# Optimization experiments

Hardware: AMD Instinct MI355X
Metric: run time of the kernel (lower is better)

## Reference

```python
import jax, jax.numpy as jnp
import numpy as np

NUM_SEGMENTS = 100000  # number of cycle slots (max cycle id + 1)


def setup_inputs() -> dict:
    key = jax.random.key(0)
    k1, k2, k3 = jax.random.split(key, 3)
    x = jax.random.randint(k1, (100000,), 0, 22, dtype=jnp.int64)
    atom_to_cycle = jax.random.randint(k2, (2, 600000), 0, NUM_SEGMENTS, dtype=jnp.int64)
    emb_weight = jax.random.normal(k3, (22, 128), dtype=jnp.float32)  # Embedding(22, hidden_dim)
    return {"x": x, "atom_to_cycle": atom_to_cycle, "emb_weight": emb_weight}


def reference(x, atom_to_cycle, emb_weight):
    # x: [N] int atom codes; atom_to_cycle: [2, E]; emb_weight: [22, D]
    h = emb_weight[x]                       # [N, D] embedding lookup
    gathered = h[atom_to_cycle[0]]          # [E, D] gather by atom index
    # scatter_sum over cycle ids -> [NUM_SEGMENTS, D]
    out = jax.ops.segment_sum(gathered, atom_to_cycle[1], num_segments=NUM_SEGMENTS)
    return out
```

## Files before the change

### kernel.cpp

```cpp
#include <hip/hip_runtime.h>
#include <stdint.h>

#define KCODES 22
#define KW     12

typedef int   int4v   __attribute__((ext_vector_type(4)));
typedef float float4v __attribute__((ext_vector_type(4)));

#define BSHIFT   8
#define BROWS    256
#define MAXBUCK  1024
#define EPT2     8
#define CHUNK2   2048
#define CAP      32
#define BCAP     4096
#define EPT      8
#define CHUNK    2048

__global__ __launch_bounds__(256) void bin_dense(
        const int* __restrict__ a2c, const int* __restrict__ x,
        uint16_t* __restrict__ cntm, uint16_t* __restrict__ bins,
        int E, int nbuck, int nchunk) {
    __shared__ uint32_t lcnt[MAXBUCK];
    const int tid = threadIdx.x;
    const int cb  = blockIdx.x;
    for (int b = tid; b < nbuck; b += 256) lcnt[b] = 0;
    __syncthreads();

    const int base = cb * CHUNK2 + tid * EPT2;
    int atoms[EPT2] __attribute__((aligned(16)));
    int cycs[EPT2]  __attribute__((aligned(16)));
    if (((E & 3) == 0) && (base + EPT2 <= E)) {
#pragma unroll
        for (int q = 0; q < EPT2 / 4; ++q) {
            *(int4v*)(atoms + 4 * q) = __builtin_nontemporal_load((const int4v*)(a2c + base) + q);
            *(int4v*)(cycs + 4 * q)  = __builtin_nontemporal_load((const int4v*)(a2c + E + base) + q);
        }
    } else {
#pragma unroll
        for (int j = 0; j < EPT2; ++j) {
            int ei = base + j;
            atoms[j] = (ei < E) ? a2c[ei] : 0;
            cycs[j]  = (ei < E) ? a2c[E + ei] : -1;
        }
    }

#pragma unroll
    for (int j = 0; j < EPT2; ++j) {
        if (cycs[j] >= 0) {
            uint32_t code = (uint32_t)x[atoms[j]];
            uint32_t b    = (uint32_t)cycs[j] >> BSHIFT;
            uint32_t rk   = atomicAdd(&lcnt[b], 1u);
            uint16_t val  = (uint16_t)((((uint32_t)cycs[j] & (BROWS - 1)) << 5) | code);
            if (rk < CAP)
                bins[((size_t)b * nchunk + cb) * CAP + rk] = val;
        }
    }
    __syncthreads();

    for (int b = tid; b < nbuck; b += 256)
        cntm[(size_t)b * nchunk + cb] = (uint16_t)lcnt[b];
}

__global__ __launch_bounds__(256) void hist_expand2(
        const uint16_t* __restrict__ cntm, const uint16_t* __restrict__ bins,
        const float* __restrict__ emb, float* __restrict__ out,
        int num_seg, int nchunk) {
    __shared__ uint32_t hist[BROWS * KW];
    __shared__ uint16_t lc[512];
    const int tid = threadIdx.x;
    const int b   = blockIdx.x;
    const int d4  = tid & 31;
    const int sub = tid >> 5;

    float4v e[KCODES];
#pragma unroll
    for (int k = 0; k < KCODES; ++k)
        e[k] = ((const float4v*)emb)[k * 32 + d4];

    for (int i = tid; i < BROWS * KW; i += 256) hist[i] = 0;
    for (int i = tid; i < nchunk; i += 256) lc[i] = cntm[(size_t)b * nchunk + i];
    __syncthreads();

    const uint16_t* bb = bins + (size_t)b * nchunk * CAP;
    for (int i = tid; i < nchunk; i += 256) {
        int c = lc[i]; if (c > CAP) c = CAP;
        const uint16_t* cell = bb + (size_t)i * CAP;
        for (int j = 0; j < c; ++j) {
            uint32_t v = cell[j];
            atomicAdd(&hist[(v >> 5) * KW + ((v & 31u) >> 1)], 1u << ((v & 1u) << 4));
        }
    }
    __syncthreads();

    for (int r = sub; r < BROWS; r += 8) {
        int cyc = b * BROWS + r;
        if (cyc >= num_seg) break;
        const uint4* hrow = (const uint4*)&hist[r * KW];
        uint4 w0 = hrow[0], w1 = hrow[1], w2 = hrow[2];
        uint32_t wv[12] = {w0.x, w0.y, w0.z, w0.w,
                           w1.x, w1.y, w1.z, w1.w,
                           w2.x, w2.y, w2.z, w2.w};
        float4v acc = (float4v)(0.f);
#pragma unroll
        for (int w = 0; w < 11; ++w) {
            float c0 = (float)(wv[w] & 0xFFFFu);
            float c1 = (float)(wv[w] >> 16);
            float4v e0 = e[2 * w], e1 = e[2 * w + 1];
            acc.x = fmaf(c1, e1.x, fmaf(c0, e0.x, acc.x));
            acc.y = fmaf(c1, e1.y, fmaf(c0, e0.y, acc.y));
            acc.z = fmaf(c1, e1.z, fmaf(c0, e0.z, acc.z));
            acc.w = fmaf(c1, e1.w, fmaf(c0, e0.w, acc.w));
        }
        __builtin_nontemporal_store(acc, &((float4v*)out)[(size_t)cyc * 32 + d4]);
    }
}

__global__ __launch_bounds__(256) void bin_edges(
        const int* __restrict__ a2c, const int* __restrict__ x,
        uint32_t* __restrict__ gcur, uint16_t* __restrict__ binsA,
        int E, int nbuck) {
    __shared__ uint32_t lcnt[MAXBUCK];
    __shared__ uint32_t lbase[MAXBUCK];
    const int tid = threadIdx.x;
    for (int b = tid; b < nbuck; b += 256) lcnt[b] = 0;
    __syncthreads();

    const int base = blockIdx.x * CHUNK + tid * EPT;
    int atoms[EPT] __attribute__((aligned(16)));
    int cycs[EPT]  __attribute__((aligned(16)));
    if (((E & 3) == 0) && (base + EPT <= E)) {
        *(int4v*)(atoms + 0) = __builtin_nontemporal_load((const int4v*)(a2c + base));
        *(int4v*)(atoms + 4) = __builtin_nontemporal_load((const int4v*)(a2c + base) + 1);
        *(int4v*)(cycs + 0)  = __builtin_nontemporal_load((const int4v*)(a2c + E + base));
        *(int4v*)(cycs + 4)  = __builtin_nontemporal_load((const int4v*)(a2c + E + base) + 1);
    } else {
#pragma unroll
        for (int j = 0; j < EPT; ++j) {
            int ei = base + j;
            atoms[j] = (ei < E) ? a2c[ei] : 0;
            cycs[j]  = (ei < E) ? a2c[E + ei] : -1;
        }
    }

    uint16_t val[EPT], bk[EPT], rk[EPT];
#pragma unroll
    for (int j = 0; j < EPT; ++j) {
        if (cycs[j] >= 0) {
            uint32_t code = (uint32_t)x[atoms[j]];
            uint32_t b    = (uint32_t)cycs[j] >> BSHIFT;
            bk[j]  = (uint16_t)b;
            rk[j]  = (uint16_t)atomicAdd(&lcnt[b], 1u);
            val[j] = (uint16_t)((((uint32_t)cycs[j] & (BROWS - 1)) << 5) | code);
        } else {
            bk[j] = 0xFFFFu;
        }
    }
    __syncthreads();

    for (int b = tid; b < nbuck; b += 256) {
        uint32_t c = lcnt[b];
        lbase[b] = c ? atomicAdd(&gcur[b], c) : 0u;
    }
    __syncthreads();

#pragma unroll
    for (int j = 0; j < EPT; ++j) {
        if (bk[j] != 0xFFFFu) {
            uint32_t idx = lbase[bk[j]] + rk[j];
            if (idx < BCAP)
                binsA[(size_t)bk[j] * BCAP + idx] = val[j];
        }
    }
}

__global__ __launch_bounds__(256) void hist_expand(
        const uint32_t* __restrict__ gcur, const uint16_t* __restrict__ binsA,
        const float* __restrict__ emb, float* __restrict__ out, int num_seg) {
    __shared__ uint32_t hist[BROWS * KW];
    const int tid = threadIdx.x;
    const int b   = blockIdx.x;
    const int d4  = tid & 31;
    const int sub = tid >> 5;

    float4v e[KCODES];
#pragma unroll
    for (int k = 0; k < KCODES; ++k)
        e[k] = ((const float4v*)emb)[k * 32 + d4];

    for (int i = tid; i < BROWS * KW; i += 256) hist[i] = 0;
    __syncthreads();

    int n = gcur[b]; if (n > BCAP) n = BCAP;
    const uint16_t* bb = binsA + (size_t)b * BCAP;
    for (int i = tid; i < n; i += 256) {
        uint32_t v = bb[i];
        atomicAdd(&hist[(v >> 5) * KW + ((v & 31u) >> 1)], 1u << ((v & 1u) << 4));
    }
    __syncthreads();

    for (int r = sub; r < BROWS; r += 8) {
        int cyc = b * BROWS + r;
        if (cyc >= num_seg) break;
        const uint4* hrow = (const uint4*)&hist[r * KW];
        uint4 w0 = hrow[0], w1 = hrow[1], w2 = hrow[2];
        uint32_t wv[12] = {w0.x, w0.y, w0.z, w0.w,
                           w1.x, w1.y, w1.z, w1.w,
                           w2.x, w2.y, w2.z, w2.w};
        float4v acc = (float4v)(0.f);
#pragma unroll
        for (int w = 0; w < 11; ++w) {
            float c0 = (float)(wv[w] & 0xFFFFu);
            float c1 = (float)(wv[w] >> 16);
            float4v e0 = e[2 * w], e1 = e[2 * w + 1];
            acc.x = fmaf(c1, e1.x, fmaf(c0, e0.x, acc.x));
            acc.y = fmaf(c1, e1.y, fmaf(c0, e0.y, acc.y));
            acc.z = fmaf(c1, e1.z, fmaf(c0, e0.z, acc.z));
            acc.w = fmaf(c1, e1.w, fmaf(c0, e0.w, acc.w));
        }
        __builtin_nontemporal_store(acc, &((float4v*)out)[(size_t)cyc * 32 + d4]);
    }
}

__global__ void zero_out_f4(float4* __restrict__ out, int n4) {
    int i = blockIdx.x * blockDim.x + threadIdx.x;
    if (i < n4) out[i] = make_float4(0.f, 0.f, 0.f, 0.f);
}

__global__ void scatter_edges(const int* __restrict__ a2c,
                              const int* __restrict__ x,
                              const float* __restrict__ emb,
                              float* __restrict__ out, int E) {
    int t = blockIdx.x * blockDim.x + threadIdx.x;
    int e = t >> 5;
    int d = (t & 31) * 4;
    if (e < E) {
        int atom = a2c[e];
        int cyc  = a2c[E + e];
        int code = x[atom];
        const float4 ev = ((const float4*)emb)[code * 32 + (d >> 2)];
        float* o = out + (size_t)cyc * 128 + d;
        atomicAdd(o + 0, ev.x);
        atomicAdd(o + 1, ev.y);
        atomicAdd(o + 2, ev.z);
        atomicAdd(o + 3, ev.w);
    }
}

extern "C" void kernel_launch(void* const* d_in, const int* in_sizes, int n_in,
                              void* d_out, int out_size, void* d_ws, size_t ws_size,
                              hipStream_t stream) {
    const int*   x    = (const int*)d_in[0];
    const int*   a2c  = (const int*)d_in[1];
    const float* emb  = (const float*)d_in[2];
    float*       out  = (float*)d_out;

    const int E       = in_sizes[1] / 2;
    const int D       = in_sizes[2] / KCODES;
    const int num_seg = out_size / D;

    const int nbuck  = (num_seg + BROWS - 1) >> BSHIFT;
    const int nchunk = (E + CHUNK2 - 1) / CHUNK2;

    const size_t cntm_bytes = (size_t)nbuck * nchunk * sizeof(uint16_t);
    const size_t bins_off   = (cntm_bytes + 65535) & ~(size_t)65535;
    const size_t need_dense = bins_off + (size_t)nbuck * nchunk * CAP * sizeof(uint16_t);
    const size_t curA_bytes = (size_t)nbuck * sizeof(uint32_t);
    const size_t binsA_off  = (curA_bytes + 65535) & ~(size_t)65535;
    const size_t need_A     = binsA_off + (size_t)nbuck * BCAP * sizeof(uint16_t);

    if (nbuck <= MAXBUCK && nchunk <= 512 && ws_size >= need_dense) {
        uint16_t* cntm = (uint16_t*)d_ws;
        uint16_t* bins = (uint16_t*)((char*)d_ws + bins_off);
        bin_dense<<<nchunk, 256, 0, stream>>>(a2c, x, cntm, bins, E, nbuck, nchunk);
        hist_expand2<<<nbuck, 256, 0, stream>>>(cntm, bins, emb, out, num_seg, nchunk);
    } else if (nbuck <= MAXBUCK && ws_size >= need_A) {
        uint32_t* gcur  = (uint32_t*)d_ws;
        uint16_t* binsA = (uint16_t*)((char*)d_ws + binsA_off);
        (void)hipMemsetAsync(gcur, 0, curA_bytes, stream);
        int blocks1 = (E + CHUNK - 1) / CHUNK;
        bin_edges<<<blocks1, 256, 0, stream>>>(a2c, x, gcur, binsA, E, nbuck);
        hist_expand<<<nbuck, 256, 0, stream>>>(gcur, binsA, emb, out, num_seg);
    } else {
        int n4 = out_size / 4;
        zero_out_f4<<<(n4 + 255) / 256, 256, 0, stream>>>((float4*)out, n4);
        long long threads = (long long)E * 32;
        int blocks = (int)((threads + 255) / 256);
        scatter_edges<<<blocks, 256, 0, stream>>>(a2c, x, emb, out, E);
    }
    (void)n_in; (void)D;
}
```

Measured before the change: 97.28 us.

## Stage bins in LDS and write 64-byte cells with inline counts

The binning kernel now collects each bucket's entries in a shared-memory cell whose first slot holds the count, then writes whole cells to global memory as coalesced 16-byte stores. The separate count matrix goes away. The histogram kernel reads each cell with uint4 loads and an unrolled count-guarded chain instead of scalar 16-bit loads. This is meant to replace scattered 2-byte global writes and reads with wide coalesced transfers. In exchange it always writes full 64-byte cells, lowers per-cell capacity by one, and raises LDS use in bin_dense.

```diff
diff --git a/kernel.cpp b/kernel.cpp
--- a/kernel.cpp
+++ b/kernel.cpp
@@ -9,19 +9,21 @@
 
 #define BSHIFT   8
 #define BROWS    256
+#define DBUCK    512
 #define MAXBUCK  1024
 #define EPT2     8
 #define CHUNK2   2048
-#define CAP      32
+#define CAPW     32
 #define BCAP     4096
 #define EPT      8
 #define CHUNK    2048
 
 __global__ __launch_bounds__(256) void bin_dense(
         const int* __restrict__ a2c, const int* __restrict__ x,
-        uint16_t* __restrict__ cntm, uint16_t* __restrict__ bins,
+        uint16_t* __restrict__ bins,
         int E, int nbuck, int nchunk) {
-    __shared__ uint32_t lcnt[MAXBUCK];
+    __shared__ uint32_t lcnt[DBUCK];
+    __shared__ uint16_t lcell[DBUCK * CAPW];
     const int tid = threadIdx.x;
     const int cb  = blockIdx.x;
     for (int b = tid; b < nbuck; b += 256) lcnt[b] = 0;
@@ -51,23 +53,31 @@
             uint32_t code = (uint32_t)x[atoms[j]];
             uint32_t b    = (uint32_t)cycs[j] >> BSHIFT;
             uint32_t rk   = atomicAdd(&lcnt[b], 1u);
-            uint16_t val  = (uint16_t)((((uint32_t)cycs[j] & (BROWS - 1)) << 5) | code);
-            if (rk < CAP)
-                bins[((size_t)b * nchunk + cb) * CAP + rk] = val;
-        }
-    }
-    __syncthreads();
-
-    for (int b = tid; b < nbuck; b += 256)
-        cntm[(size_t)b * nchunk + cb] = (uint16_t)lcnt[b];
+            if (rk < CAPW - 1)
+                lcell[b * CAPW + 1 + rk] =
+                    (uint16_t)((((uint32_t)cycs[j] & (BROWS - 1)) << 5) | code);
+        }
+    }
+    __syncthreads();
+
+    for (int b = tid; b < nbuck; b += 256) {
+        uint32_t c = lcnt[b];
+        lcell[b * CAPW] = (uint16_t)(c < CAPW ? c : (CAPW - 1));
+    }
+    __syncthreads();
+
+    const int nseg = nbuck * 4;
+    for (int s = tid; s < nseg; s += 256) {
+        int b = s >> 2, seg = s & 3;
+        ((uint4*)bins)[((size_t)b * nchunk + cb) * 4 + seg] = ((const uint4*)lcell)[s];
+    }
 }
 
 __global__ __launch_bounds__(256) void hist_expand2(
-        const uint16_t* __restrict__ cntm, const uint16_t* __restrict__ bins,
+        const uint16_t* __restrict__ bins,
         const float* __restrict__ emb, float* __restrict__ out,
         int num_seg, int nchunk) {
     __shared__ uint32_t hist[BROWS * KW];
-    __shared__ uint16_t lc[512];
     const int tid = threadIdx.x;
     const int b   = blockIdx.x;
     const int d4  = tid & 31;
@@ -79,18 +89,59 @@
         e[k] = ((const float4v*)emb)[k * 32 + d4];
 
     for (int i = tid; i < BROWS * KW; i += 256) hist[i] = 0;
-    for (int i = tid; i < nchunk; i += 256) lc[i] = cntm[(size_t)b * nchunk + i];
-    __syncthreads();
-
-    const uint16_t* bb = bins + (size_t)b * nchunk * CAP;
+    __syncthreads();
+
+#define H(v) atomicAdd(&hist[((v) >> 5) * KW + (((v) & 31u) >> 1)], 1u << (((v) & 1u) << 4))
+    const uint4* cells = (const uint4*)bins;
     for (int i = tid; i < nchunk; i += 256) {
-        int c = lc[i]; if (c > CAP) c = CAP;
-        const uint16_t* cell = bb + (size_t)i * CAP;
-        for (int j = 0; j < c; ++j) {
-            uint32_t v = cell[j];
-            atomicAdd(&hist[(v >> 5) * KW + ((v & 31u) >> 1)], 1u << ((v & 1u) << 4));
-        }
-    }
+        const uint4* cp = cells + ((size_t)b * nchunk + i) * 4;
+        uint4 q0 = cp[0];
+        int c = (int)(q0.x & 0xFFFFu);
+        if (c > 0) {
+            uint32_t v;
+            v = q0.x >> 16;     H(v);
+            if (c > 1) { v = q0.y & 0xFFFFu; H(v); }
+            if (c > 2) { v = q0.y >> 16;     H(v); }
+            if (c > 3) { v = q0.z & 0xFFFFu; H(v); }
+            if (c > 4) { v = q0.z >> 16;     H(v); }
+            if (c > 5) { v = q0.w & 0xFFFFu; H(v); }
+            if (c > 6) { v = q0.w >> 16;     H(v); }
+            if (c > 7) {
+                uint4 q1 = cp[1];
+                v = q1.x & 0xFFFFu; H(v);
+                if (c > 8)  { v = q1.x >> 16;     H(v); }
+                if (c > 9)  { v = q1.y & 0xFFFFu; H(v); }
+                if (c > 10) { v = q1.y >> 16;     H(v); }
+                if (c > 11) { v = q1.z & 0xFFFFu; H(v); }
+                if (c > 12) { v = q1.z >> 16;     H(v); }
+                if (c > 13) { v = q1.w & 0xFFFFu; H(v); }
+                if (c > 14) { v = q1.w >> 16;     H(v); }
+                if (c > 15) {
+                    uint4 q2 = cp[2];
+                    v = q2.x & 0xFFFFu; H(v);
+                    if (c > 16) { v = q2.x >> 16;     H(v); }
+                    if (c > 17) { v = q2.y & 0xFFFFu; H(v); }
+                    if (c > 18) { v = q2.y >> 16;     H(v); }
+                    if (c > 19) { v = q2.z & 0xFFFFu; H(v); }
+                    if (c > 20) { v = q2.z >> 16;     H(v); }
+                    if (c > 21) { v = q2.w & 0xFFFFu; H(v); }
+                    if (c > 22) { v = q2.w >> 16;     H(v); }
+                    if (c > 23) {
+                        uint4 q3 = cp[3];
+                        v = q3.x & 0xFFFFu; H(v);
+                        if (c > 24) { v = q3.x >> 16;     H(v); }
+                        if (c > 25) { v = q3.y & 0xFFFFu; H(v); }
+                        if (c > 26) { v = q3.y >> 16;     H(v); }
+                        if (c > 27) { v = q3.z & 0xFFFFu; H(v); }
+                        if (c > 28) { v = q3.z >> 16;     H(v); }
+                        if (c > 29) { v = q3.w & 0xFFFFu; H(v); }
+                        if (c > 30) { v = q3.w >> 16;     H(v); }
+                    }
+                }
+            }
+        }
+    }
+#undef H
     __syncthreads();
 
     for (int r = sub; r < BROWS; r += 8) {
@@ -262,18 +313,17 @@
     const int nbuck  = (num_seg + BROWS - 1) >> BSHIFT;
     const int nchunk = (E + CHUNK2 - 1) / CHUNK2;
 
-    const size_t cntm_bytes = (size_t)nbuck * nchunk * sizeof(uint16_t);
-    const size_t bins_off   = (cntm_bytes + 65535) & ~(size_t)65535;
-    const size_t need_dense = bins_off + (size_t)nbuck * nchunk * CAP * sizeof(uint16_t);
+    const size_t need_dense = (size_t)nbuck * nchunk * CAPW * sizeof(uint16_t);
     const size_t curA_bytes = (size_t)nbuck * sizeof(uint32_t);
     const size_t binsA_off  = (curA_bytes + 65535) & ~(size_t)65535;
     const size_t need_A     = binsA_off + (size_t)nbuck * BCAP * sizeof(uint16_t);
 
-    if (nbuck <= MAXBUCK && nchunk <= 512 && ws_size >= need_dense) {
-        uint16_t* cntm = (uint16_t*)d_ws;
-        uint16_t* bins = (uint16_t*)((char*)d_ws + bins_off);
-        bin_dense<<<nchunk, 256, 0, stream>>>(a2c, x, cntm, bins, E, nbuck, nchunk);
-        hist_expand2<<<nbuck, 256, 0, stream>>>(cntm, bins, emb, out, num_seg, nchunk);
+    const bool ws_aligned = (((uintptr_t)d_ws) & 15) == 0;
+
+    if (nbuck <= DBUCK && ws_aligned && ws_size >= need_dense) {
+        uint16_t* bins = (uint16_t*)d_ws;
+        bin_dense<<<nchunk, 256, 0, stream>>>(a2c, x, bins, E, nbuck, nchunk);
+        hist_expand2<<<nbuck, 256, 0, stream>>>(bins, emb, out, num_seg, nchunk);
     } else if (nbuck <= MAXBUCK && ws_size >= need_A) {
         uint32_t* gcur  = (uint32_t*)d_ws;
         uint16_t* binsA = (uint16_t*)((char*)d_ws + binsA_off);
```

Result: faster. 93.26 us (-4.1%).
